# Kernel optimization log

Hardware: AMD Instinct MI355X
Metric: run time of the kernel (lower is better)

## Reference

```python
import jax, jax.numpy as jnp
import numpy as np

B, N, C, K = 2, 8192, 128, 16

def _mlp2(h, W1, b1, W2, b2):
    return jax.nn.relu(h @ W1 + b1) @ W2 + b2

def setup_inputs() -> dict:
    key = jax.random.key(0)
    ks = jax.random.split(key, 20)
    s = lambda d: 1.0 / np.sqrt(d)
    inp = {
        "x": jax.random.normal(ks[0], (B, N, C), jnp.float32),
        "position": jax.random.normal(ks[1], (B, N, 3), jnp.float32),
        "Wq": jax.random.normal(ks[2], (C, C), jnp.float32) * s(C),
        "bq": jnp.zeros((C,), jnp.float32),
        "Wk": jax.random.normal(ks[3], (C, C), jnp.float32) * s(C),
        "bk": jnp.zeros((C,), jnp.float32),
        "Wv": jax.random.normal(ks[4], (C, C), jnp.float32) * s(C),
        "bv": jnp.zeros((C,), jnp.float32),
        "Wp1": jax.random.normal(ks[5], (3, C), jnp.float32) * s(3),
        "bp1": jnp.zeros((C,), jnp.float32),
        "Wp2": jax.random.normal(ks[6], (C, C), jnp.float32) * s(C),
        "bp2": jnp.zeros((C,), jnp.float32),
        "Wg1": jax.random.normal(ks[7], (C, C), jnp.float32) * s(C),
        "bg1": jnp.zeros((C,), jnp.float32),
        "Wg2": jax.random.normal(ks[8], (C, C), jnp.float32) * s(C),
        "bg2": jnp.zeros((C,), jnp.float32),
    }
    return inp

def reference(x, position, Wq, bq, Wk, bk, Wv, bv, Wp1, bp1, Wp2, bp2, Wg1, bg1, Wg2, bg2):
    # kNN via squared pairwise distances (monotone in cdist, same topk indices)
    p2 = jnp.sum(position * position, axis=-1)                       # (B,N)
    d2 = p2[:, :, None] + p2[:, None, :] - 2.0 * jnp.einsum("bnd,bmd->bnm", position, position)
    _, idx = jax.lax.top_k(-d2, K)                                    # (B,N,K) nearest (incl self)

    gather = jax.vmap(lambda arr, i: arr[i])                          # per-batch fancy gather
    neighbors = gather(x, idx)                                        # (B,N,K,C)
    pos_nb = gather(position, idx)                                    # (B,N,K,3)

    q = x @ Wq + bq                                                   # (B,N,C)
    k = neighbors @ Wk + bk                                           # (B,N,K,C)
    v = neighbors @ Wv + bv                                           # (B,N,K,C)

    # positional MLP only at gathered pairs (same math as all-pairs-then-gather)
    rel = position[:, :, None, :] - pos_nb                            # (B,N,K,3)
    pe = _mlp2(rel, Wp1, bp1, Wp2, bp2)                               # (B,N,K,C)

    scale = 1.0 / jnp.sqrt(jnp.float32(C))
    attn = (q[:, :, None, :] - k + pe) * scale
    attn = _mlp2(attn, Wg1, bg1, Wg2, bg2)
    attn = jax.nn.softmax(attn, axis=2)                               # softmax over K neighbors
    out = jnp.sum(attn * (v + pe), axis=2)                            # (B,N,C)
    return out
```

## Files before the change

### kernel.cpp

```cpp
#include <hip/hip_runtime.h>
#include <hip/hip_bf16.h>
#include <stdint.h>

#define NPTS 8192
#define CDIM 128
#define KNNK 16
#define WELEMF 16384
#define SCALE 0.08838834764831845f
#define FLDS_BYTES 74752
#define GRES 16
#define NCELL (GRES*GRES*GRES)

typedef __attribute__((ext_vector_type(4))) float f32x4;
typedef __attribute__((ext_vector_type(8))) short s16x8;

__device__ __forceinline__ unsigned short to_bf16(float f){
  union { __hip_bfloat16 h; unsigned short u; } v;
  v.h = __float2bfloat16(f);
  return v.u;
}

__device__ __forceinline__ s16x8 cvt8(const float* p){
  float4 lo = *(const float4*)p;
  float4 hi = *(const float4*)(p + 4);
  s16x8 f;
  f[0]=(short)to_bf16(lo.x); f[1]=(short)to_bf16(lo.y);
  f[2]=(short)to_bf16(lo.z); f[3]=(short)to_bf16(lo.w);
  f[4]=(short)to_bf16(hi.x); f[5]=(short)to_bf16(hi.y);
  f[6]=(short)to_bf16(hi.z); f[7]=(short)to_bf16(hi.w);
  return f;
}

__device__ __forceinline__ unsigned mapf_u(unsigned s){
  return s ^ (0x80000000u | (unsigned)(((int)s) >> 31));
}
__device__ __forceinline__ float unmapf_u(unsigned u){
  unsigned r = (u & 0x80000000u) ? (u ^ 0x80000000u) : ~u;
  return __uint_as_float(r);
}

__global__ __launch_bounds__(256) void zero_init_kernel(int* __restrict__ counts,
                                                        unsigned* __restrict__ bbox)
{
  int t = blockIdx.x*256 + threadIdx.x;
  if (t < 2*NCELL) counts[t] = 0;
  if (t < 12) bbox[t] = ((t % 6) < 3) ? 0xFFFFFFFFu : 0u;
}

__global__ __launch_bounds__(256) void prep_kernel(
    const float* __restrict__ Wq, const float* __restrict__ Wk,
    const float* __restrict__ Wv, const float* __restrict__ Wp2,
    const float* __restrict__ Wg1, const float* __restrict__ Wg2,
    const float* __restrict__ pos,
    unsigned short* __restrict__ wt, float4* __restrict__ pos4,
    unsigned* __restrict__ bbox)
{
  int t = blockIdx.x*256 + threadIdx.x;
  if (t < 6*WELEMF){
    int w = t >> 14, f = t & (WELEMF-1);
    int i = f & 7, ln = (f >> 3) & 63, kkct = f >> 9;
    int kk = kkct & 3, ct = kkct >> 2;
    int kdim = kk*32 + (ln >> 4)*8 + i, col = ct*16 + (ln & 15);
    const float* src = (w==0)?Wq:(w==1)?Wk:(w==2)?Wv:(w==3)?Wp2:(w==4)?Wg1:Wg2;
    float v = src[kdim*CDIM + col];
    if (w == 1) v = -v;
    wt[t] = to_bf16(v);
  } else {
    int m = t - 6*WELEMF;
    float xx = pos[m*3+0], yy = pos[m*3+1], zz = pos[m*3+2];
    float p2 = __fadd_rn(__fadd_rn(__fmul_rn(xx,xx), __fmul_rn(yy,yy)), __fmul_rn(zz,zz));
    pos4[m] = make_float4(xx, yy, zz, p2);
    unsigned mnx = mapf_u(__float_as_uint(xx)), mny = mapf_u(__float_as_uint(yy)), mnz = mapf_u(__float_as_uint(zz));
    unsigned mxx = mnx, mxy = mny, mxz = mnz;
#pragma unroll
    for (int off = 1; off < 64; off <<= 1){
      mnx = min(mnx, (unsigned)__shfl_xor((int)mnx, off));
      mny = min(mny, (unsigned)__shfl_xor((int)mny, off));
      mnz = min(mnz, (unsigned)__shfl_xor((int)mnz, off));
      mxx = max(mxx, (unsigned)__shfl_xor((int)mxx, off));
      mxy = max(mxy, (unsigned)__shfl_xor((int)mxy, off));
      mxz = max(mxz, (unsigned)__shfl_xor((int)mxz, off));
    }
    if ((threadIdx.x & 63) == 0){
      int b = m >> 13;
      atomicMin(&bbox[b*6+0], mnx); atomicMin(&bbox[b*6+1], mny); atomicMin(&bbox[b*6+2], mnz);
      atomicMax(&bbox[b*6+3], mxx); atomicMax(&bbox[b*6+4], mxy); atomicMax(&bbox[b*6+5], mxz);
    }
  }
}

__global__ __launch_bounds__(256) void bin_count_kernel(
    const float4* __restrict__ pos4, const unsigned* __restrict__ bbox,
    int* __restrict__ counts, int* __restrict__ cellId)
{
  int m = blockIdx.x*256 + threadIdx.x;
  int b = m >> 13;
  float4 p = pos4[m];
  float lox = unmapf_u(bbox[b*6+0]), loy = unmapf_u(bbox[b*6+1]), loz = unmapf_u(bbox[b*6+2]);
  float hix = unmapf_u(bbox[b*6+3]), hiy = unmapf_u(bbox[b*6+4]), hiz = unmapf_u(bbox[b*6+5]);
  int ix = min(GRES-1, max(0, (int)((p.x - lox) * ((float)GRES/(hix-lox)))));
  int iy = min(GRES-1, max(0, (int)((p.y - loy) * ((float)GRES/(hiy-loy)))));
  int iz = min(GRES-1, max(0, (int)((p.z - loz) * ((float)GRES/(hiz-loz)))));
  int cid = (iz*GRES + iy)*GRES + ix;
  cellId[m] = cid;
  atomicAdd(&counts[b*NCELL + cid], 1);
}

__global__ __launch_bounds__(1024) void scan_kernel(
    const int* __restrict__ counts, int* __restrict__ starts, int* __restrict__ cursor)
{
  __shared__ int part[1024];
  int b = blockIdx.x, t = threadIdx.x;
  const int* c = counts + b*NCELL;
  int* s = starts + b*(NCELL+1);
  int* cur = cursor + b*NCELL;
  int base = t*4, sum = 0;
  for (int i = 0; i < 4; ++i) sum += c[base+i];
  part[t] = sum; __syncthreads();
  for (int off = 1; off < 1024; off <<= 1){
    int v = (t >= off) ? part[t-off] : 0;
    __syncthreads();
    part[t] += v;
    __syncthreads();
  }
  int run = (t > 0) ? part[t-1] : 0;
  for (int i = 0; i < 4; ++i){ int cc = c[base+i]; s[base+i] = run; cur[base+i] = run; run += cc; }
  if (t == 1023) s[NCELL] = run;
}

__global__ __launch_bounds__(256) void scatter_kernel(
    const float4* __restrict__ pos4, const int* __restrict__ cellId,
    int* __restrict__ cursor, float4* __restrict__ spos4)
{
  int m = blockIdx.x*256 + threadIdx.x;
  int b = m >> 13;
  float4 p = pos4[m];
  int dst = atomicAdd(&cursor[b*NCELL + cellId[m]], 1);
  spos4[(b<<13) + dst] = make_float4(p.x, p.y, p.z, __uint_as_float((unsigned)(m & (NPTS-1))));
}

__global__ __launch_bounds__(256) void knn_grid_kernel(
    const float4* __restrict__ spos4, const int* __restrict__ starts,
    const unsigned* __restrict__ bbox, int* __restrict__ idxout)
{
  const int tid = threadIdx.x, lane = tid & 63;
  const int sub = lane >> 4, sl = lane & 15, gbase = sub*16;
  const int w = tid >> 6;
  const int g = blockIdx.x*16 + w*4 + sub;
  const int b = g >> 13, n = g & (NPTS-1);
  const float4* sp = spos4 + ((size_t)b<<13);
  const int*    st = starts + b*(NCELL+1);

  const float4 q4 = sp[n];
  const int orig = __float_as_int(q4.w);
  const float qx = q4.x, qy = q4.y, qz = q4.z;
  const float q2 = __fadd_rn(__fadd_rn(__fmul_rn(qx,qx), __fmul_rn(qy,qy)), __fmul_rn(qz,qz));

  float lox = unmapf_u(bbox[b*6+0]), loy = unmapf_u(bbox[b*6+1]), loz = unmapf_u(bbox[b*6+2]);
  float hix = unmapf_u(bbox[b*6+3]), hiy = unmapf_u(bbox[b*6+4]), hiz = unmapf_u(bbox[b*6+5]);
  float cwx = (hix-lox)*(1.0f/GRES), cwy = (hiy-loy)*(1.0f/GRES), cwz = (hiz-loz)*(1.0f/GRES);
  int cx = min(GRES-1, max(0, (int)((qx - lox) * ((float)GRES/(hix-lox)))));
  int cy = min(GRES-1, max(0, (int)((qy - loy) * ((float)GRES/(hiy-loy)))));
  int cz = min(GRES-1, max(0, (int)((qz - loz) * ((float)GRES/(hiz-loz)))));

  unsigned khi = 0xFFFFFFFFu, klo = 0xFFFFFFFFu;
  float Tf = __builtin_inff();

  auto insert = [&](unsigned ihi, unsigned ilo){
    unsigned phi = (unsigned)__builtin_amdgcn_update_dpp(0, (int)khi, 0x111, 0xF, 0xF, false);
    unsigned plo = (unsigned)__builtin_amdgcn_update_dpp(0, (int)klo, 0x111, 0xF, 0xF, false);
    bool gt  = (khi > ihi) || (khi == ihi && klo > ilo);
    bool pgt = (sl != 0) && ((phi > ihi) || (phi == ihi && plo > ilo));
    khi = gt ? (pgt ? phi : ihi) : khi;
    klo = gt ? (pgt ? plo : ilo) : klo;
  };
  auto updT = [&](){
    unsigned t15 = (unsigned)__shfl((int)khi, gbase + 15);
    Tf = (t15 >= 0xFF800000u) ? __builtin_inff() : unmapf_u(t15);
  };

  bool gdone = false;
  for (int R = 1; R <= GRES-1; ++R){
    const bool first = (R == 1);
    const int per = 8*R, w1 = 2*R-1;
    const int ntask = first ? 9 : (per + 2*w1*w1);
    for (int tb = 0; tb < ntask; tb += 16){
      int t = tb + sl;
      int dy = 0, dz = 0, gx0 = 0, gx1 = -1;
      bool valid = (!gdone) && (t < ntask);
      if (first){
        if (valid){ dy = t % 3 - 1; dz = t / 3 - 1; }
        gx0 = max(cx-1, 0); gx1 = min(cx+1, GRES-1);
      } else if (valid){
        if (t < per){
          int s2 = 2*(2*R+1);
          if (t < s2){ dz = (t < 2*R+1) ? -R : R; dy = t % (2*R+1) - R; }
          else { int u = t - s2; dy = (u & 1) ? R : -R; dz = (u >> 1) - (R-1); }
          gx0 = max(cx-R, 0); gx1 = min(cx+R, GRES-1);
        } else {
          int i = t - per, ri = i >> 1;
          dy = ri % w1 - (R-1); dz = ri / w1 - (R-1);
          int gx = cx + ((i & 1) ? R : -R);
          gx0 = gx; gx1 = gx;
          valid = gx >= 0 && gx <= GRES-1;
        }
      }
      int gy = cy + dy, gz = cz + dz;
      valid = valid && gy >= 0 && gy < GRES && gz >= 0 && gz < GRES && gx0 <= gx1;
      int s0 = 0, s1 = 0;
      if (valid){ int cb = (gz*GRES + gy)*GRES; s0 = st[cb + gx0]; s1 = st[cb + gx1 + 1]; }
      unsigned long long bal = __ballot(valid && (s1 > s0));
      unsigned cm = (unsigned)((bal >> gbase) & 0xFFFFull);
      while (__any(cm != 0)){
        bool act = (cm != 0);
        int srow = act ? __builtin_ctz(cm) : 0;
        if (act) cm &= cm - 1;
        int cs = __shfl(s0, gbase + srow);
        int ce = __shfl(s1, gbase + srow);
        if (!act){ cs = 0; ce = 0; }
        for (int p0 = cs; p0 < ce; p0 += 16){
          int mm = p0 + sl;
          bool v = mm < ce;
          float4 c = v ? sp[mm] : make_float4(0.f,0.f,0.f,0.f);
          float c2  = __fadd_rn(__fadd_rn(__fmul_rn(c.x,c.x), __fmul_rn(c.y,c.y)), __fmul_rn(c.z,c.z));
          float dot = __builtin_fmaf(c.z, qz, __builtin_fmaf(c.y, qy, __fmul_rn(c.x, qx)));
          float d2  = __fsub_rn(__fadd_rn(q2, c2), __fadd_rn(dot, dot));
          int oi = __float_as_int(c.w);
          bool ins = v && (d2 <= Tf);
          unsigned long long ib = __ballot(ins);
          unsigned im = (unsigned)((ib >> gbase) & 0xFFFFull);
          if (__any(im != 0)){
            while (__any(im != 0)){
              bool a2 = (im != 0);
              int s = a2 ? __builtin_ctz(im) : 0;
              if (a2) im &= im - 1;
              unsigned dvb = (unsigned)__shfl((int)__float_as_uint(d2), gbase + s);
              int ov = __shfl(oi, gbase + s);
              if (a2) insert(mapf_u(dvb), (unsigned)ov);
            }
            updT();
          }
        }
      }
    }
    const float big = 1e30f;
    float dxlo = (cx-R <= 0)      ? big : (qx - (lox + (float)(cx-R)*cwx));
    float dxhi = (cx+R >= GRES-1) ? big : ((lox + (float)(cx+R+1)*cwx) - qx);
    float dylo = (cy-R <= 0)      ? big : (qy - (loy + (float)(cy-R)*cwy));
    float dyhi = (cy+R >= GRES-1) ? big : ((loy + (float)(cy+R+1)*cwy) - qy);
    float dzlo = (cz-R <= 0)      ? big : (qz - (loz + (float)(cz-R)*cwz));
    float dzhi = (cz+R >= GRES-1) ? big : ((loz + (float)(cz+R+1)*cwz) - qz);
    float dmin = fminf(fminf(fminf(dxlo,dxhi), fminf(dylo,dyhi)), fminf(dzlo,dzhi));
    bool full = dmin >= 1e29f;
    dmin = fmaxf(dmin, 0.0f);
    float dmin2 = dmin*dmin;
    bool stop = full || (Tf + 1e-4f + Tf*1e-5f < dmin2);
    gdone = gdone || stop;
    if (__all(gdone)) break;
  }
  idxout[(((size_t)b<<13) + orig)*KNNK + sl] = (int)klo;
}

__global__ __launch_bounds__(256, 2) void fused_kernel(
    const float* __restrict__ x, const float* __restrict__ pos,
    const float* __restrict__ bq, const float* __restrict__ bk,
    const float* __restrict__ bv, const float* __restrict__ Wp1,
    const float* __restrict__ bp1, const float* __restrict__ bp2,
    const float* __restrict__ bg1, const float* __restrict__ bg2,
    const int* __restrict__ idxws, const unsigned short* __restrict__ wt,
    float* __restrict__ out)
{
  extern __shared__ char smem[];
  char* Sbase = smem;
  char* Tbase = smem + 32768;
  float* blds = (float*)(smem + 65536);
  float* q_lds = (float*)(smem + 70656);

  const int tid = threadIdx.x;
  const int lane = tid & 63, w = tid >> 6;
  const int r = lane & 15, grp = lane >> 4;
  const int pbase = blockIdx.x * 8;
  const int b = pbase >> 13;

  auto gll = [&](int s, char* dst){
#pragma unroll
    for (int k = 0; k < 8; ++k){
      int c = w*8 + k;
      unsigned short* g = const_cast<unsigned short*>(wt) + (size_t)s*WELEMF + c*512 + lane*8;
      __builtin_amdgcn_global_load_lds(
        (const __attribute__((address_space(1))) void*)g,
        (__attribute__((address_space(3))) void*)(dst + c*1024), 16, 0, 0);
    }
  };
  auto ldS = [&](int ct, int kk) -> s16x8 {
    return *(const s16x8*)&((unsigned short*)Sbase)[((ct*4 + kk)*64 + lane)*8];
  };
  auto ldT = [&](int ct, int kk) -> s16x8 {
    return *(const s16x8*)&((unsigned short*)Tbase)[((ct*4 + kk)*64 + lane)*8];
  };

  gll(0, Sbase);
  gll(3, Tbase);

  for (int e = tid; e < 1280; e += 256){
    float v;
    if      (e < 128)  v = bq[e];
    else if (e < 256)  v = bk[e-128];
    else if (e < 384)  v = bv[e-256];
    else if (e < 512)  v = bp2[e-384];
    else if (e < 640)  v = bg1[e-512];
    else if (e < 768)  v = bg2[e-640];
    else if (e < 896)  v = bp1[e-768];
    else               v = Wp1[e-896];
    blds[e] = v;
  }
  int nbr[2]; float relx[2], rely[2], relz[2];
#pragma unroll
  for (int j = 0; j < 2; ++j){
    int gp = pbase + w*2 + j;
    nbr[j] = idxws[(size_t)gp*KNNK + r];
    const float* pq = pos + (size_t)gp*3;
    const float* pn = pos + ((size_t)b*NPTS + nbr[j])*3;
    relx[j] = pq[0]-pn[0]; rely[j] = pq[1]-pn[1]; relz[j] = pq[2]-pn[2];
  }
  s16x8 qa[4];
  {
    const float* xr = x + (size_t)(pbase + (r & 7))*CDIM;
#pragma unroll
    for (int kk = 0; kk < 4; ++kk) qa[kk] = cvt8(xr + kk*32 + grp*8);
  }
  __syncthreads();

  {
    f32x4 qacc[2] = { {0.f,0.f,0.f,0.f}, {0.f,0.f,0.f,0.f} };
#pragma unroll
    for (int c2 = 0; c2 < 2; ++c2){
      int ct = w*2 + c2;
#pragma unroll
      for (int kk = 0; kk < 4; ++kk)
        qacc[c2] = __builtin_amdgcn_mfma_f32_16x16x32_bf16(qa[kk], ldS(ct,kk), qacc[c2], 0,0,0);
    }
#pragma unroll
    for (int c2 = 0; c2 < 2; ++c2){
      int col = (w*2+c2)*16 + r;
#pragma unroll
      for (int jj = 0; jj < 4; ++jj){
        int row = grp*4 + jj;
        if (row < 8) q_lds[row*CDIM + col] = qacc[c2][jj] + blds[col];
      }
    }
  }
  s16x8 pf[2][4];
#pragma unroll
  for (int j = 0; j < 2; ++j)
#pragma unroll
    for (int kk = 0; kk < 4; ++kk){
      s16x8 f;
#pragma unroll
      for (int i = 0; i < 8; ++i){
        int kc = kk*32 + grp*8 + i;
        float s = relx[j]*blds[896+kc] + rely[j]*blds[1024+kc] + relz[j]*blds[1152+kc] + blds[768+kc];
        f[i] = (short)to_bf16(fmaxf(s, 0.f));
      }
      pf[j][kk] = f;
    }
  __syncthreads();
  gll(1, Sbase);

  f32x4 at[2][8], av[2][8];
#pragma unroll
  for (int j=0;j<2;++j)
#pragma unroll
    for (int ct=0;ct<8;++ct) at[j][ct] = (f32x4){0.f,0.f,0.f,0.f};
#pragma unroll
  for (int ct=0;ct<8;++ct)
#pragma unroll
    for (int kk=0;kk<4;++kk){
      s16x8 bw = ldT(ct,kk);
#pragma unroll
      for (int j=0;j<2;++j)
        at[j][ct] = __builtin_amdgcn_mfma_f32_16x16x32_bf16(pf[j][kk], bw, at[j][ct], 0,0,0);
    }
  s16x8 nf[2][4];
#pragma unroll
  for (int j=0;j<2;++j)
#pragma unroll
    for (int kk=0;kk<4;++kk)
      nf[j][kk] = cvt8(x + ((size_t)b*NPTS + nbr[j])*CDIM + kk*32 + grp*8);

  __syncthreads();
  gll(2, Tbase);
#pragma unroll
  for (int j=0;j<2;++j)
#pragma unroll
    for (int ct=0;ct<8;++ct) av[j][ct] = at[j][ct];
#pragma unroll
  for (int ct=0;ct<8;++ct)
#pragma unroll
    for (int kk=0;kk<4;++kk){
      s16x8 bw = ldS(ct,kk);
#pragma unroll
      for (int j=0;j<2;++j) at[j][ct] = __builtin_amdgcn_mfma_f32_16x16x32_bf16(nf[j][kk], bw, at[j][ct], 0,0,0);
    }
  __syncthreads();
  gll(4, Sbase);
#pragma unroll
  for (int ct=0;ct<8;++ct)
#pragma unroll
    for (int kk=0;kk<4;++kk){
      s16x8 bw = ldT(ct,kk);
#pragma unroll
      for (int j=0;j<2;++j) av[j][ct] = __builtin_amdgcn_mfma_f32_16x16x32_bf16(nf[j][kk], bw, av[j][ct], 0,0,0);
    }
#pragma unroll
  for (int j=0;j<2;++j){
    int prow = (w*2+j)*CDIM;
#pragma unroll
    for (int ct=0;ct<8;++ct){
      int col = ct*16+r;
      float add = q_lds[prow+col] + blds[384+col] - blds[128+col];
#pragma unroll
      for (int jj=0;jj<4;++jj) at[j][ct][jj] = (at[j][ct][jj] + add)*SCALE;
    }
  }
  __syncthreads();

#pragma unroll
  for (int j=0;j<2;++j){
    unsigned short* tj = (unsigned short*)Tbase + (w*2+j)*2048;
#pragma unroll
    for (int ct=0;ct<8;++ct){
      int base = (ct>>1)*512 + ((ct&1)*2 + (r>>3))*128 + (r&7);
#pragma unroll
      for (int jj=0;jj<4;++jj)
        tj[base + (grp*4+jj)*8] = to_bf16(at[j][ct][jj]);
    }
  }
  s16x8 tf[2][4];
#pragma unroll
  for (int j=0;j<2;++j){
    const unsigned short* tj = (const unsigned short*)Tbase + (w*2+j)*2048;
#pragma unroll
    for (int kk=0;kk<4;++kk)
      tf[j][kk] = *(const s16x8*)&tj[(kk*64 + lane)*8];
  }
  f32x4 hacc[2][8];
#pragma unroll
  for (int j=0;j<2;++j)
#pragma unroll
    for (int ct=0;ct<8;++ct) hacc[j][ct] = (f32x4){0.f,0.f,0.f,0.f};
#pragma unroll
  for (int ct=0;ct<8;++ct)
#pragma unroll
    for (int kk=0;kk<4;++kk){
      s16x8 bw = ldS(ct,kk);
#pragma unroll
      for (int j=0;j<2;++j)
        hacc[j][ct] = __builtin_amdgcn_mfma_f32_16x16x32_bf16(tf[j][kk], bw, hacc[j][ct], 0,0,0);
    }
  __syncthreads();
  gll(5, Sbase);
#pragma unroll
  for (int j=0;j<2;++j){
    unsigned short* tj = (unsigned short*)Tbase + (w*2+j)*2048;
#pragma unroll
    for (int ct=0;ct<8;++ct){
      int base = (ct>>1)*512 + ((ct&1)*2 + (r>>3))*128 + (r&7);
      int col = ct*16+r; float bb = blds[512+col];
#pragma unroll
      for (int jj=0;jj<4;++jj)
        tj[base + (grp*4+jj)*8] = to_bf16(fmaxf(hacc[j][ct][jj]+bb, 0.f));
    }
  }
  s16x8 hf[2][4];
#pragma unroll
  for (int j=0;j<2;++j){
    const unsigned short* tj = (const unsigned short*)Tbase + (w*2+j)*2048;
#pragma unroll
    for (int kk=0;kk<4;++kk)
      hf[j][kk] = *(const s16x8*)&tj[(kk*64 + lane)*8];
  }
  __syncthreads();
  f32x4 gacc[2][8];
#pragma unroll
  for (int j=0;j<2;++j)
#pragma unroll
    for (int ct=0;ct<8;++ct) gacc[j][ct] = (f32x4){0.f,0.f,0.f,0.f};
#pragma unroll
  for (int ct=0;ct<8;++ct)
#pragma unroll
    for (int kk=0;kk<4;++kk){
      s16x8 bw = ldS(ct,kk);
#pragma unroll
      for (int j=0;j<2;++j)
        gacc[j][ct] = __builtin_amdgcn_mfma_f32_16x16x32_bf16(hf[j][kk], bw, gacc[j][ct], 0,0,0);
    }
#pragma unroll
  for (int j=0;j<2;++j){
#pragma unroll
    for (int ct=0;ct<8;++ct){
      int col = ct*16+r;
      float gb = blds[640+col];
      float g0v = gacc[j][ct][0]+gb, g1v = gacc[j][ct][1]+gb;
      float g2v = gacc[j][ct][2]+gb, g3v = gacc[j][ct][3]+gb;
      float mx = fmaxf(fmaxf(g0v,g1v), fmaxf(g2v,g3v));
      mx = fmaxf(mx, __shfl_xor(mx,16));
      mx = fmaxf(mx, __shfl_xor(mx,32));
      float e0=__expf(g0v-mx), e1=__expf(g1v-mx), e2=__expf(g2v-mx), e3=__expf(g3v-mx);
      float vb = blds[256+col] + blds[384+col];
      float ss = e0+e1+e2+e3;
      float oo = e0*(av[j][ct][0]+vb) + e1*(av[j][ct][1]+vb)
               + e2*(av[j][ct][2]+vb) + e3*(av[j][ct][3]+vb);
      ss += __shfl_xor(ss,16); ss += __shfl_xor(ss,32);
      oo += __shfl_xor(oo,16); oo += __shfl_xor(oo,32);
      if (grp == 0) out[(size_t)(pbase + w*2 + j)*CDIM + col] = oo/ss;
    }
  }
}

extern "C" void kernel_launch(void* const* d_in, const int* in_sizes, int n_in,
                              void* d_out, int out_size, void* d_ws, size_t ws_size,
                              hipStream_t stream)
{
  const float* x    = (const float*)d_in[0];
  const float* pos  = (const float*)d_in[1];
  const float* Wq   = (const float*)d_in[2];
  const float* bq   = (const float*)d_in[3];
  const float* Wk   = (const float*)d_in[4];
  const float* bk   = (const float*)d_in[5];
  const float* Wv   = (const float*)d_in[6];
  const float* bv   = (const float*)d_in[7];
  const float* Wp1  = (const float*)d_in[8];
  const float* bp1  = (const float*)d_in[9];
  const float* Wp2  = (const float*)d_in[10];
  const float* bp2  = (const float*)d_in[11];
  const float* Wg1  = (const float*)d_in[12];
  const float* bg1  = (const float*)d_in[13];
  const float* Wg2  = (const float*)d_in[14];
  const float* bg2  = (const float*)d_in[15];
  float* out = (float*)d_out;

  char* ws = (char*)d_ws;
  int*            idxs   = (int*)ws;
  unsigned short* wt     = (unsigned short*)(ws + 1048576);
  float4*         pos4   = (float4*)(ws + 1257472);
  float4*         spos4  = (float4*)(ws + 1519616);
  int*            cellId = (int*)(ws + 1847296);
  int*            counts = (int*)(ws + 1912832);
  int*            starts = (int*)(ws + 2174976);
  int*            cursor = (int*)(ws + 2437376);
  unsigned*       bbox   = (unsigned*)(ws + 2699520);

  hipFuncSetAttribute((const void*)fused_kernel,
                      hipFuncAttributeMaxDynamicSharedMemorySize, FLDS_BYTES);

  zero_init_kernel<<<32, 256, 0, stream>>>(counts, bbox);
  prep_kernel<<<448, 256, 0, stream>>>(Wq, Wk, Wv, Wp2, Wg1, Wg2, pos, wt, pos4, bbox);
  bin_count_kernel<<<64, 256, 0, stream>>>(pos4, bbox, counts, cellId);
  scan_kernel<<<2, 1024, 0, stream>>>(counts, starts, cursor);
  scatter_kernel<<<64, 256, 0, stream>>>(pos4, cellId, cursor, spos4);
  knn_grid_kernel<<<1024, 256, 0, stream>>>(spos4, starts, bbox, idxs);
  fused_kernel<<<2048, 256, FLDS_BYTES, stream>>>(x, pos, bq, bk, bv, Wp1, bp1, bp2,
                                                  bg1, bg2, idxs, wt, out);
}
```

Baseline: 211.4 us.

## Fuse grid kNN search into the attention kernel via shared-memory neighbor indices

Removes the separate knn_grid_kernel launch. Two waves of each fused_kernel block now run the grid kNN search for the block's 8 query points and write the indices into a small new LDS region, which the whole block reads after a barrier. This drops one kernel launch and the global write and read of the neighbor-index buffer. In exchange, the other two waves sit idle during the search, and the search's long latency now runs serially inside the low-occupancy fused kernel.

New measurement: 398.3 us. 88.4% more time.

```diff
diff --git a/kernel.cpp b/kernel.cpp
--- a/kernel.cpp
+++ b/kernel.cpp
@@ -7,7 +7,7 @@
 #define KNNK 16
 #define WELEMF 16384
 #define SCALE 0.08838834764831845f
-#define FLDS_BYTES 74752
+#define FLDS_BYTES 75264
 #define GRES 16
 #define NCELL (GRES*GRES*GRES)
 
@@ -139,135 +139,15 @@
   spos4[(b<<13) + dst] = make_float4(p.x, p.y, p.z, __uint_as_float((unsigned)(m & (NPTS-1))));
 }
 
-__global__ __launch_bounds__(256) void knn_grid_kernel(
-    const float4* __restrict__ spos4, const int* __restrict__ starts,
-    const unsigned* __restrict__ bbox, int* __restrict__ idxout)
-{
-  const int tid = threadIdx.x, lane = tid & 63;
-  const int sub = lane >> 4, sl = lane & 15, gbase = sub*16;
-  const int w = tid >> 6;
-  const int g = blockIdx.x*16 + w*4 + sub;
-  const int b = g >> 13, n = g & (NPTS-1);
-  const float4* sp = spos4 + ((size_t)b<<13);
-  const int*    st = starts + b*(NCELL+1);
-
-  const float4 q4 = sp[n];
-  const int orig = __float_as_int(q4.w);
-  const float qx = q4.x, qy = q4.y, qz = q4.z;
-  const float q2 = __fadd_rn(__fadd_rn(__fmul_rn(qx,qx), __fmul_rn(qy,qy)), __fmul_rn(qz,qz));
-
-  float lox = unmapf_u(bbox[b*6+0]), loy = unmapf_u(bbox[b*6+1]), loz = unmapf_u(bbox[b*6+2]);
-  float hix = unmapf_u(bbox[b*6+3]), hiy = unmapf_u(bbox[b*6+4]), hiz = unmapf_u(bbox[b*6+5]);
-  float cwx = (hix-lox)*(1.0f/GRES), cwy = (hiy-loy)*(1.0f/GRES), cwz = (hiz-loz)*(1.0f/GRES);
-  int cx = min(GRES-1, max(0, (int)((qx - lox) * ((float)GRES/(hix-lox)))));
-  int cy = min(GRES-1, max(0, (int)((qy - loy) * ((float)GRES/(hiy-loy)))));
-  int cz = min(GRES-1, max(0, (int)((qz - loz) * ((float)GRES/(hiz-loz)))));
-
-  unsigned khi = 0xFFFFFFFFu, klo = 0xFFFFFFFFu;
-  float Tf = __builtin_inff();
-
-  auto insert = [&](unsigned ihi, unsigned ilo){
-    unsigned phi = (unsigned)__builtin_amdgcn_update_dpp(0, (int)khi, 0x111, 0xF, 0xF, false);
-    unsigned plo = (unsigned)__builtin_amdgcn_update_dpp(0, (int)klo, 0x111, 0xF, 0xF, false);
-    bool gt  = (khi > ihi) || (khi == ihi && klo > ilo);
-    bool pgt = (sl != 0) && ((phi > ihi) || (phi == ihi && plo > ilo));
-    khi = gt ? (pgt ? phi : ihi) : khi;
-    klo = gt ? (pgt ? plo : ilo) : klo;
-  };
-  auto updT = [&](){
-    unsigned t15 = (unsigned)__shfl((int)khi, gbase + 15);
-    Tf = (t15 >= 0xFF800000u) ? __builtin_inff() : unmapf_u(t15);
-  };
-
-  bool gdone = false;
-  for (int R = 1; R <= GRES-1; ++R){
-    const bool first = (R == 1);
-    const int per = 8*R, w1 = 2*R-1;
-    const int ntask = first ? 9 : (per + 2*w1*w1);
-    for (int tb = 0; tb < ntask; tb += 16){
-      int t = tb + sl;
-      int dy = 0, dz = 0, gx0 = 0, gx1 = -1;
-      bool valid = (!gdone) && (t < ntask);
-      if (first){
-        if (valid){ dy = t % 3 - 1; dz = t / 3 - 1; }
-        gx0 = max(cx-1, 0); gx1 = min(cx+1, GRES-1);
-      } else if (valid){
-        if (t < per){
-          int s2 = 2*(2*R+1);
-          if (t < s2){ dz = (t < 2*R+1) ? -R : R; dy = t % (2*R+1) - R; }
-          else { int u = t - s2; dy = (u & 1) ? R : -R; dz = (u >> 1) - (R-1); }
-          gx0 = max(cx-R, 0); gx1 = min(cx+R, GRES-1);
-        } else {
-          int i = t - per, ri = i >> 1;
-          dy = ri % w1 - (R-1); dz = ri / w1 - (R-1);
-          int gx = cx + ((i & 1) ? R : -R);
-          gx0 = gx; gx1 = gx;
-          valid = gx >= 0 && gx <= GRES-1;
-        }
-      }
-      int gy = cy + dy, gz = cz + dz;
-      valid = valid && gy >= 0 && gy < GRES && gz >= 0 && gz < GRES && gx0 <= gx1;
-      int s0 = 0, s1 = 0;
-      if (valid){ int cb = (gz*GRES + gy)*GRES; s0 = st[cb + gx0]; s1 = st[cb + gx1 + 1]; }
-      unsigned long long bal = __ballot(valid && (s1 > s0));
-      unsigned cm = (unsigned)((bal >> gbase) & 0xFFFFull);
-      while (__any(cm != 0)){
-        bool act = (cm != 0);
-        int srow = act ? __builtin_ctz(cm) : 0;
-        if (act) cm &= cm - 1;
-        int cs = __shfl(s0, gbase + srow);
-        int ce = __shfl(s1, gbase + srow);
-        if (!act){ cs = 0; ce = 0; }
-        for (int p0 = cs; p0 < ce; p0 += 16){
-          int mm = p0 + sl;
-          bool v = mm < ce;
-          float4 c = v ? sp[mm] : make_float4(0.f,0.f,0.f,0.f);
-          float c2  = __fadd_rn(__fadd_rn(__fmul_rn(c.x,c.x), __fmul_rn(c.y,c.y)), __fmul_rn(c.z,c.z));
-          float dot = __builtin_fmaf(c.z, qz, __builtin_fmaf(c.y, qy, __fmul_rn(c.x, qx)));
-          float d2  = __fsub_rn(__fadd_rn(q2, c2), __fadd_rn(dot, dot));
-          int oi = __float_as_int(c.w);
-          bool ins = v && (d2 <= Tf);
-          unsigned long long ib = __ballot(ins);
-          unsigned im = (unsigned)((ib >> gbase) & 0xFFFFull);
-          if (__any(im != 0)){
-            while (__any(im != 0)){
-              bool a2 = (im != 0);
-              int s = a2 ? __builtin_ctz(im) : 0;
-              if (a2) im &= im - 1;
-              unsigned dvb = (unsigned)__shfl((int)__float_as_uint(d2), gbase + s);
-              int ov = __shfl(oi, gbase + s);
-              if (a2) insert(mapf_u(dvb), (unsigned)ov);
-            }
-            updT();
-          }
-        }
-      }
-    }
-    const float big = 1e30f;
-    float dxlo = (cx-R <= 0)      ? big : (qx - (lox + (float)(cx-R)*cwx));
-    float dxhi = (cx+R >= GRES-1) ? big : ((lox + (float)(cx+R+1)*cwx) - qx);
-    float dylo = (cy-R <= 0)      ? big : (qy - (loy + (float)(cy-R)*cwy));
-    float dyhi = (cy+R >= GRES-1) ? big : ((loy + (float)(cy+R+1)*cwy) - qy);
-    float dzlo = (cz-R <= 0)      ? big : (qz - (loz + (float)(cz-R)*cwz));
-    float dzhi = (cz+R >= GRES-1) ? big : ((loz + (float)(cz+R+1)*cwz) - qz);
-    float dmin = fminf(fminf(fminf(dxlo,dxhi), fminf(dylo,dyhi)), fminf(dzlo,dzhi));
-    bool full = dmin >= 1e29f;
-    dmin = fmaxf(dmin, 0.0f);
-    float dmin2 = dmin*dmin;
-    bool stop = full || (Tf + 1e-4f + Tf*1e-5f < dmin2);
-    gdone = gdone || stop;
-    if (__all(gdone)) break;
-  }
-  idxout[(((size_t)b<<13) + orig)*KNNK + sl] = (int)klo;
-}
-
 __global__ __launch_bounds__(256, 2) void fused_kernel(
     const float* __restrict__ x, const float* __restrict__ pos,
     const float* __restrict__ bq, const float* __restrict__ bk,
     const float* __restrict__ bv, const float* __restrict__ Wp1,
     const float* __restrict__ bp1, const float* __restrict__ bp2,
     const float* __restrict__ bg1, const float* __restrict__ bg2,
-    const int* __restrict__ idxws, const unsigned short* __restrict__ wt,
+    const unsigned short* __restrict__ wt,
+    const float4* __restrict__ pos4, const float4* __restrict__ spos4,
+    const int* __restrict__ starts, const unsigned* __restrict__ bboxg,
     float* __restrict__ out)
 {
   extern __shared__ char smem[];
@@ -275,6 +155,7 @@
   char* Tbase = smem + 32768;
   float* blds = (float*)(smem + 65536);
   float* q_lds = (float*)(smem + 70656);
+  int* nbrLds = (int*)(smem + 74752);
 
   const int tid = threadIdx.x;
   const int lane = tid & 63, w = tid >> 6;
@@ -314,22 +195,139 @@
     else               v = Wp1[e-896];
     blds[e] = v;
   }
-  int nbr[2]; float relx[2], rely[2], relz[2];
-#pragma unroll
-  for (int j = 0; j < 2; ++j){
-    int gp = pbase + w*2 + j;
-    nbr[j] = idxws[(size_t)gp*KNNK + r];
-    const float* pq = pos + (size_t)gp*3;
-    const float* pn = pos + ((size_t)b*NPTS + nbr[j])*3;
-    relx[j] = pq[0]-pn[0]; rely[j] = pq[1]-pn[1]; relz[j] = pq[2]-pn[2];
-  }
   s16x8 qa[4];
   {
     const float* xr = x + (size_t)(pbase + (r & 7))*CDIM;
 #pragma unroll
     for (int kk = 0; kk < 4; ++kk) qa[kk] = cvt8(xr + kk*32 + grp*8);
   }
-  __syncthreads();
+
+  if (w < 2){
+    const int sub = grp, sl = r, gbase = sub*16;
+    const int j8 = w*4 + sub;
+    const int n = (pbase + j8) & (NPTS-1);
+    const float4* sp = spos4 + ((size_t)b<<13);
+    const int*    st = starts + b*(NCELL+1);
+
+    const float4 q4 = pos4[((size_t)b<<13) + n];
+    const float qx = q4.x, qy = q4.y, qz = q4.z;
+    const float q2 = q4.w;
+
+    float lox = unmapf_u(bboxg[b*6+0]), loy = unmapf_u(bboxg[b*6+1]), loz = unmapf_u(bboxg[b*6+2]);
+    float hix = unmapf_u(bboxg[b*6+3]), hiy = unmapf_u(bboxg[b*6+4]), hiz = unmapf_u(bboxg[b*6+5]);
+    float cwx = (hix-lox)*(1.0f/GRES), cwy = (hiy-loy)*(1.0f/GRES), cwz = (hiz-loz)*(1.0f/GRES);
+    int cx = min(GRES-1, max(0, (int)((qx - lox) * ((float)GRES/(hix-lox)))));
+    int cy = min(GRES-1, max(0, (int)((qy - loy) * ((float)GRES/(hiy-loy)))));
+    int cz = min(GRES-1, max(0, (int)((qz - loz) * ((float)GRES/(hiz-loz)))));
+
+    unsigned khi = 0xFFFFFFFFu, klo = 0xFFFFFFFFu;
+    float Tf = __builtin_inff();
+
+    auto insert = [&](unsigned ihi, unsigned ilo){
+      unsigned phi = (unsigned)__builtin_amdgcn_update_dpp(0, (int)khi, 0x111, 0xF, 0xF, false);
+      unsigned plo = (unsigned)__builtin_amdgcn_update_dpp(0, (int)klo, 0x111, 0xF, 0xF, false);
+      bool gt  = (khi > ihi) || (khi == ihi && klo > ilo);
+      bool pgt = (sl != 0) && ((phi > ihi) || (phi == ihi && plo > ilo));
+      khi = gt ? (pgt ? phi : ihi) : khi;
+      klo = gt ? (pgt ? plo : ilo) : klo;
+    };
+    auto updT = [&](){
+      unsigned t15 = (unsigned)__shfl((int)khi, gbase + 15);
+      Tf = (t15 >= 0xFF800000u) ? __builtin_inff() : unmapf_u(t15);
+    };
+
+    bool gdone = false;
+    for (int R = 1; R <= GRES-1; ++R){
+      const bool first = (R == 1);
+      const int per = 8*R, w1 = 2*R-1;
+      const int ntask = first ? 9 : (per + 2*w1*w1);
+      for (int tb = 0; tb < ntask; tb += 16){
+        int t = tb + sl;
+        int dy = 0, dz = 0, gx0 = 0, gx1 = -1;
+        bool valid = (!gdone) && (t < ntask);
+        if (first){
+          if (valid){ dy = t % 3 - 1; dz = t / 3 - 1; }
+          gx0 = max(cx-1, 0); gx1 = min(cx+1, GRES-1);
+        } else if (valid){
+          if (t < per){
+            int s2 = 2*(2*R+1);
+            if (t < s2){ dz = (t < 2*R+1) ? -R : R; dy = t % (2*R+1) - R; }
+            else { int u = t - s2; dy = (u & 1) ? R : -R; dz = (u >> 1) - (R-1); }
+            gx0 = max(cx-R, 0); gx1 = min(cx+R, GRES-1);
+          } else {
+            int i = t - per, ri = i >> 1;
+            dy = ri % w1 - (R-1); dz = ri / w1 - (R-1);
+            int gx = cx + ((i & 1) ? R : -R);
+            gx0 = gx; gx1 = gx;
+            valid = gx >= 0 && gx <= GRES-1;
+          }
+        }
+        int gy = cy + dy, gz = cz + dz;
+        valid = valid && gy >= 0 && gy < GRES && gz >= 0 && gz < GRES && gx0 <= gx1;
+        int s0 = 0, s1 = 0;
+        if (valid){ int cb = (gz*GRES + gy)*GRES; s0 = st[cb + gx0]; s1 = st[cb + gx1 + 1]; }
+        unsigned long long bal = __ballot(valid && (s1 > s0));
+        unsigned cm = (unsigned)((bal >> gbase) & 0xFFFFull);
+        while (__any(cm != 0)){
+          bool act = (cm != 0);
+          int srow = act ? __builtin_ctz(cm) : 0;
+          if (act) cm &= cm - 1;
+          int cs = __shfl(s0, gbase + srow);
+          int ce = __shfl(s1, gbase + srow);
+          if (!act){ cs = 0; ce = 0; }
+          for (int p0 = cs; p0 < ce; p0 += 16){
+            int mm = p0 + sl;
+            bool v = mm < ce;
+            float4 c = v ? sp[mm] : make_float4(0.f,0.f,0.f,0.f);
+            float c2  = __fadd_rn(__fadd_rn(__fmul_rn(c.x,c.x), __fmul_rn(c.y,c.y)), __fmul_rn(c.z,c.z));
+            float dot = __builtin_fmaf(c.z, qz, __builtin_fmaf(c.y, qy, __fmul_rn(c.x, qx)));
+            float d2  = __fsub_rn(__fadd_rn(q2, c2), __fadd_rn(dot, dot));
+            int oi = __float_as_int(c.w);
+            bool ins = v && (d2 <= Tf);
+            unsigned long long ib = __ballot(ins);
+            unsigned im = (unsigned)((ib >> gbase) & 0xFFFFull);
+            if (__any(im != 0)){
+              while (__any(im != 0)){
+                bool a2 = (im != 0);
+                int s = a2 ? __builtin_ctz(im) : 0;
+                if (a2) im &= im - 1;
+                unsigned dvb = (unsigned)__shfl((int)__float_as_uint(d2), gbase + s);
+                int ov = __shfl(oi, gbase + s);
+                if (a2) insert(mapf_u(dvb), (unsigned)ov);
+              }
+              updT();
+            }
+          }
+        }
+      }
+      const float big = 1e30f;
+      float dxlo = (cx-R <= 0)      ? big : (qx - (lox + (float)(cx-R)*cwx));
+      float dxhi = (cx+R >= GRES-1) ? big : ((lox + (float)(cx+R+1)*cwx) - qx);
+      float dylo = (cy-R <= 0)      ? big : (qy - (loy + (float)(cy-R)*cwy));
+      float dyhi = (cy+R >= GRES-1) ? big : ((loy + (float)(cy+R+1)*cwy) - qy);
+      float dzlo = (cz-R <= 0)      ? big : (qz - (loz + (float)(cz-R)*cwz));
+      float dzhi = (cz+R >= GRES-1) ? big : ((loz + (float)(cz+R+1)*cwz) - qz);
+      float dmin = fminf(fminf(fminf(dxlo,dxhi), fminf(dylo,dyhi)), fminf(dzlo,dzhi));
+      bool full = dmin >= 1e29f;
+      dmin = fmaxf(dmin, 0.0f);
+      float dmin2 = dmin*dmin;
+      bool stop = full || (Tf + 1e-4f + Tf*1e-5f < dmin2);
+      gdone = gdone || stop;
+      if (__all(gdone)) break;
+    }
+    nbrLds[j8*16 + sl] = (int)klo;
+  }
+  __syncthreads();
+
+  int nbr[2]; float relx[2], rely[2], relz[2];
+#pragma unroll
+  for (int j = 0; j < 2; ++j){
+    int jp = w*2 + j;
+    nbr[j] = nbrLds[jp*16 + r];
+    const float* pq = pos + (size_t)(pbase + jp)*3;
+    const float* pn = pos + ((size_t)b*NPTS + nbr[j])*3;
+    relx[j] = pq[0]-pn[0]; rely[j] = pq[1]-pn[1]; relz[j] = pq[2]-pn[2];
+  }
 
   {
     f32x4 qacc[2] = { {0.f,0.f,0.f,0.f}, {0.f,0.f,0.f,0.f} };
@@ -541,7 +539,6 @@
   float* out = (float*)d_out;
 
   char* ws = (char*)d_ws;
-  int*            idxs   = (int*)ws;
   unsigned short* wt     = (unsigned short*)(ws + 1048576);
   float4*         pos4   = (float4*)(ws + 1257472);
   float4*         spos4  = (float4*)(ws + 1519616);
@@ -559,7 +556,7 @@
   bin_count_kernel<<<64, 256, 0, stream>>>(pos4, bbox, counts, cellId);
   scan_kernel<<<2, 1024, 0, stream>>>(counts, starts, cursor);
   scatter_kernel<<<64, 256, 0, stream>>>(pos4, cellId, cursor, spos4);
-  knn_grid_kernel<<<1024, 256, 0, stream>>>(spos4, starts, bbox, idxs);
   fused_kernel<<<2048, 256, FLDS_BYTES, stream>>>(x, pos, bq, bk, bv, Wp1, bp1, bp2,
-                                                  bg1, bg2, idxs, wt, out);
-}
+                                                  bg1, bg2, wt, pos4, spos4, starts,
+                                                  bbox, out);
+}
```
